# Kernel tuning notes

Measured on AMD Instinct MI355X. Metric: run time of the kernel, lower is better.

The kernel has to match this reference:

```python
import jax, jax.numpy as jnp
import numpy as np

N, M, E, H = 20000, 32, 20, 128


def _branch(nodes, rbf_edges, nbrs_idx, Wf, bf, Wfull, bfull):
    # rbf_edges: [N, M, E] -> edges: [N, M, H]
    edges = rbf_edges @ Wf + bf
    nbrs_fea = nodes[nbrs_idx]  # gather: [N, M, H]
    self_fea = jnp.broadcast_to(nodes[:, None, :], (nbrs_idx.shape[0], nbrs_idx.shape[1], nodes.shape[1]))
    total = jnp.concatenate([self_fea, edges, nbrs_fea], axis=2)  # [N, M, 3H]
    gated = total @ Wfull + bfull  # [N, M, 2H]
    filt, core = gated[..., :H], gated[..., H:]
    return jnp.sum(jax.nn.sigmoid(filt) * jax.nn.softplus(core), axis=1)  # [N, H]


def setup_inputs() -> dict:
    key = jax.random.key(0)
    ks = jax.random.split(key, 12)
    inp = {
        "nodes": jax.random.normal(ks[0], (N, H), jnp.float32),
        "che_rbf_edges": jax.random.normal(ks[1], (N, M, E), jnp.float32),
        "che_nbrs_idx": jax.random.randint(ks[2], (N, M), 0, N),
        "vdw_rbf_edges": jax.random.normal(ks[3], (N, M, E), jnp.float32),
        "vdw_nbrs_idx": jax.random.randint(ks[4], (N, M), 0, N),
        # params (nn.Linear: y = x @ W + b, W stored here as [in, out])
        "che_Wf": jax.random.normal(ks[5], (E, H), jnp.float32) / np.sqrt(E),
        "che_bf": jnp.zeros((H,), jnp.float32),
        "che_Wfull": jax.random.normal(ks[6], (3 * H, 2 * H), jnp.float32) / np.sqrt(3 * H),
        "che_bfull": jnp.zeros((2 * H,), jnp.float32),
        "vdw_Wf": jax.random.normal(ks[7], (E, H), jnp.float32) / np.sqrt(E),
        "vdw_bf": jnp.zeros((H,), jnp.float32),
        "vdw_Wfull": jax.random.normal(ks[8], (3 * H, 2 * H), jnp.float32) / np.sqrt(3 * H),
        "vdw_bfull": jnp.zeros((2 * H,), jnp.float32),
    }
    return inp


def reference(nodes, che_rbf_edges, che_nbrs_idx, vdw_rbf_edges, vdw_nbrs_idx,
              che_Wf, che_bf, che_Wfull, che_bfull,
              vdw_Wf, vdw_bf, vdw_Wfull, vdw_bfull):
    che = _branch(nodes, che_rbf_edges, che_nbrs_idx, che_Wf, che_bf, che_Wfull, che_bfull)
    vdw = _branch(nodes, vdw_rbf_edges, vdw_nbrs_idx, vdw_Wf, vdw_bf, vdw_Wfull, vdw_bfull)
    return jax.nn.softplus(nodes + che + vdw)
```

## Files before the change

kernel.cpp:

```cpp
#include <hip/hip_runtime.h>
#include <hip/hip_bf16.h>

#define NN 20000
#define MM 32
#define EE 20
#define HH 128
#define LOG2E 1.44269504088896f
#define LN2   0.69314718055995f

typedef __attribute__((ext_vector_type(8))) short bf16x8;
typedef __attribute__((ext_vector_type(4))) float f32x4;

__device__ __forceinline__ float bf_lo(unsigned int u) {
    return __uint_as_float(u << 16);
}
__device__ __forceinline__ float bf_hi(unsigned int u) {
    return __uint_as_float(u & 0xFFFF0000u);
}
__device__ __forceinline__ unsigned int pack_bf2(float lo, float hi) {
    unsigned int a = __float_as_uint(lo);
    unsigned int b = __float_as_uint(hi);
    a += 0x7FFFu + ((a >> 16) & 1u);
    b += 0x7FFFu + ((b >> 16) & 1u);
    return (a >> 16) | (b & 0xFFFF0000u);
}
__device__ __forceinline__ unsigned short bf16r(float v) {
    unsigned int u = __float_as_uint(v);
    u += 0x7FFFu + ((u >> 16) & 1u);
    return (unsigned short)(u >> 16);
}
__device__ __forceinline__ float softplusf(float x) {
    return fmaxf(x, 0.f) + __logf(1.f + __expf(-fabsf(x)));
}

__global__ void build_pfrag(const float* __restrict__ cheW,
                            const float* __restrict__ vdwW,
                            unsigned short* __restrict__ Pfrag) {
    int t = blockIdx.x * 256 + threadIdx.x;
    int i = t & 7;
    int l = (t >> 3) & 63;
    int ks = (t >> 9) & 3;
    int tile = t >> 11;
    int j = (tile & 31) * 16 + (l & 15);
    int slot = tile >> 5;
    int b = j >> 8, sec = (j >> 7) & 1, h = j & 127;
    int klocal = (l >> 4) * 8 + i;
    int row = (sec ? 256 : 0) + ks * 32 + klocal;
    const float* W = b ? vdwW : cheW;
    Pfrag[t] = bf16r(LOG2E * W[row * 256 + slot * 128 + h]);
}

__global__ void build_bfrag(const float* __restrict__ cheWf, const float* __restrict__ cheBf,
                            const float* __restrict__ cheW,  const float* __restrict__ cheBfull,
                            const float* __restrict__ vdwWf, const float* __restrict__ vdwBf,
                            const float* __restrict__ vdwW,  const float* __restrict__ vdwBfull,
                            unsigned short* __restrict__ Bfrag, float* __restrict__ biasP) {
    int t = blockIdx.x * 256 + threadIdx.x;
    int b = t >> 10, w = (t >> 9) & 1, tc = (t >> 6) & 7, l = t & 63;
    int lhi = l >> 4, llo = l & 15;
    int h = w * 64 + (tc >> 1) * 16 + llo;
    int slot = tc & 1;
    int jcol = slot * 128 + h;
    const float* Wf = b ? vdwWf : cheWf;
    const float* W  = b ? vdwW  : cheW;

    unsigned short o[8];
#pragma unroll
    for (int i = 0; i < 8; ++i) {
        int k = lhi * 8 + i;
        float a = 0.f;
        if (k < EE)
            for (int h2 = 0; h2 < 128; ++h2)
                a = fmaf(Wf[k * 128 + h2], W[(128 + h2) * 256 + jcol], a);
        o[i] = bf16r(LOG2E * a);
    }
#pragma unroll
    for (int i = 0; i < 8; ++i) Bfrag[t * 8 + i] = o[i];

    if (t < 512) {
        int bb = t >> 8, sl = (t >> 7) & 1, hh = t & 127;
        int jc = sl * 128 + hh;
        const float* bfv   = bb ? vdwBf    : cheBf;
        const float* Wb    = bb ? vdwW     : cheW;
        const float* bfull = bb ? vdwBfull : cheBfull;
        float s = bfull[jc];
        for (int h2 = 0; h2 < 128; ++h2)
            s = fmaf(bfv[h2], Wb[(128 + h2) * 256 + jc], s);
        biasP[t] = LOG2E * s;
    }
}

__global__ __launch_bounds__(256) void proj_mfma(const float* __restrict__ nodes,
                                                 const unsigned short* __restrict__ Pfrag,
                                                 unsigned int* __restrict__ P) {
    __shared__ unsigned short ln[16 * 136];
    int n0 = blockIdx.x * 16;
    int t = threadIdx.x;
    {
        int row = t >> 4, seg = t & 15;
        const float* src = &nodes[(n0 + row) * 128 + seg * 8];
        float4 v0 = *(const float4*)src;
        float4 v1 = *(const float4*)(src + 4);
        uint4 u;
        u.x = pack_bf2(v0.x, v0.y);
        u.y = pack_bf2(v0.z, v0.w);
        u.z = pack_bf2(v1.x, v1.y);
        u.w = pack_bf2(v1.z, v1.w);
        *(uint4*)&ln[row * 136 + seg * 8] = u;
    }
    __syncthreads();

    int w = t >> 6, l = t & 63, lhi = l >> 4, llo = l & 15;
    bf16x8 Af[4];
#pragma unroll
    for (int ks = 0; ks < 4; ++ks)
        Af[ks] = *(const bf16x8*)&ln[llo * 136 + ks * 32 + lhi * 8];

#pragma unroll
    for (int tp = 0; tp < 8; ++tp) {
        int ft = w * 8 + tp;
        int ct = 32 + w * 8 + tp;
        f32x4 cf = {0.f, 0.f, 0.f, 0.f};
        f32x4 cc = {0.f, 0.f, 0.f, 0.f};
#pragma unroll
        for (int ks = 0; ks < 4; ++ks) {
            bf16x8 Bf = *(const bf16x8*)&Pfrag[((ft * 4 + ks) * 64 + l) * 8];
            bf16x8 Bc = *(const bf16x8*)&Pfrag[((ct * 4 + ks) * 64 + l) * 8];
            cf = __builtin_amdgcn_mfma_f32_16x16x32_bf16(Af[ks], Bf, cf, 0, 0, 0);
            cc = __builtin_amdgcn_mfma_f32_16x16x32_bf16(Af[ks], Bc, cc, 0, 0, 0);
        }
        int j = w * 128 + tp * 16 + llo;
#pragma unroll
        for (int r = 0; r < 4; ++r)
            P[(size_t)(n0 + lhi * 4 + r) * 512 + j] = pack_bf2(cf[r], cc[r]);
    }
}

__global__ __launch_bounds__(256) void main_kernel(
    const float* __restrict__ nodes,
    const float* __restrict__ rbf_che, const int* __restrict__ idx_che,
    const float* __restrict__ rbf_vdw, const int* __restrict__ idx_vdw,
    const unsigned int* __restrict__ P,
    const unsigned short* __restrict__ Bfrag, const float* __restrict__ biasP,
    float* __restrict__ out) {
    __shared__ unsigned short sA[2 * 32 * 40];
    __shared__ int sidx[2][MM];
    int n = blockIdx.x;
    int tid = threadIdx.x;
    int w = tid >> 6, l = tid & 63;
    int lhi = l >> 4, llo = l & 15;
    int wold = w >> 1, whalf = w & 1;

    if (tid < 192) {
        int row = tid / 3, j = tid - row * 3;
        *(uint2*)&sA[row * 40 + 20 + j * 4] = make_uint2(0u, 0u);
    }
    for (int i = tid; i < 320; i += 256) {
        int b = (i >= 160) ? 1 : 0, rem = i - b * 160;
        int m = rem / 5, kq = rem - m * 5;
        const float* src = b ? rbf_vdw : rbf_che;
        float4 v = *(const float4*)&src[n * 640 + m * 20 + kq * 4];
        uint2 p;
        p.x = pack_bf2(v.x, v.y);
        p.y = pack_bf2(v.z, v.w);
        *(uint2*)&sA[(b * 32 + m) * 40 + kq * 4] = p;
    }
    if (tid < 64) {
        int b = tid >> 5, m = tid & 31;
        sidx[b][m] = (b ? idx_vdw : idx_che)[n * MM + m];
    }
    __syncthreads();

    float ps0 = 0.f, ps1 = 0.f;

#pragma unroll
    for (int b = 0; b < 2; ++b) {
        bf16x8 Af0 = *(const bf16x8*)&sA[(b * 32 + llo) * 40 + lhi * 8];
        bf16x8 Af1 = *(const bf16x8*)&sA[(b * 32 + 16 + llo) * 40 + lhi * 8];
        int4 vi0 = *(const int4*)&sidx[b][lhi * 4];
        int4 vi1 = *(const int4*)&sidx[b][16 + lhi * 4];

        int secofs = b * 256 + 128 + w * 32 + llo;
        const unsigned int* gp[8];
        gp[0] = P + (size_t)vi0.x * 512 + secofs;
        gp[1] = P + (size_t)vi0.y * 512 + secofs;
        gp[2] = P + (size_t)vi0.z * 512 + secofs;
        gp[3] = P + (size_t)vi0.w * 512 + secofs;
        gp[4] = P + (size_t)vi1.x * 512 + secofs;
        gp[5] = P + (size_t)vi1.y * 512 + secofs;
        gp[6] = P + (size_t)vi1.z * 512 + secofs;
        gp[7] = P + (size_t)vi1.w * 512 + secofs;

        const unsigned int* sp = P + (size_t)n * 512 + b * 256 + w * 32 + llo;
        const float* bfp = biasP + b * 256 + w * 32 + llo;
        const unsigned short* bb = Bfrag + (size_t)((b * 2 + wold) * 8 + whalf * 4) * 512;

#pragma unroll
        for (int ht = 0; ht < 2; ++ht) {
            bf16x8 Bff = *(const bf16x8*)(bb + ((ht * 2) * 64 + l) * 8);
            bf16x8 Bfc = *(const bf16x8*)(bb + ((ht * 2 + 1) * 64 + l) * 8);

            unsigned int su = sp[ht * 16];
            float baseF = bfp[ht * 16]       + bf_lo(su);
            float baseC = bfp[ht * 16 + 128] + bf_hi(su);

            f32x4 a0f = {baseF, baseF, baseF, baseF};
            f32x4 a0c = {baseC, baseC, baseC, baseC};
            f32x4 a1f = a0f, a1c = a0c;
            a0f = __builtin_amdgcn_mfma_f32_16x16x32_bf16(Af0, Bff, a0f, 0, 0, 0);
            a0c = __builtin_amdgcn_mfma_f32_16x16x32_bf16(Af0, Bfc, a0c, 0, 0, 0);
            a1f = __builtin_amdgcn_mfma_f32_16x16x32_bf16(Af1, Bff, a1f, 0, 0, 0);
            a1c = __builtin_amdgcn_mfma_f32_16x16x32_bf16(Af1, Bfc, a1c, 0, 0, 0);

            float s = 0.f;
#pragma unroll
            for (int r = 0; r < 4; ++r) {
                unsigned int g = gp[r][ht * 16];
                float filt = a0f[r] + bf_lo(g);
                float core = a0c[r] + bf_hi(g);
                float sg = __builtin_amdgcn_rcpf(1.f + __builtin_amdgcn_exp2f(-filt));
                float sop = fmaxf(core, 0.f) +
                            __builtin_amdgcn_logf(1.f + __builtin_amdgcn_exp2f(-fabsf(core)));
                s = fmaf(sg, sop, s);
            }
#pragma unroll
            for (int r = 0; r < 4; ++r) {
                unsigned int g = gp[4 + r][ht * 16];
                float filt = a1f[r] + bf_lo(g);
                float core = a1c[r] + bf_hi(g);
                float sg = __builtin_amdgcn_rcpf(1.f + __builtin_amdgcn_exp2f(-filt));
                float sop = fmaxf(core, 0.f) +
                            __builtin_amdgcn_logf(1.f + __builtin_amdgcn_exp2f(-fabsf(core)));
                s = fmaf(sg, sop, s);
            }
            if (ht == 0) ps0 += s;
            else ps1 += s;
        }
    }

    float v0 = ps0;
    v0 += __shfl_xor(v0, 16);
    v0 += __shfl_xor(v0, 32);
    float v1 = ps1;
    v1 += __shfl_xor(v1, 16);
    v1 += __shfl_xor(v1, 32);

    if (lhi < 2) {
        int h = w * 32 + lhi * 16 + llo;
        float res = lhi ? v1 : v0;
        float x = nodes[n * 128 + h] + LN2 * res;
        out[n * 128 + h] = softplusf(x);
    }
}

extern "C" void kernel_launch(void* const* d_in, const int* in_sizes, int n_in,
                              void* d_out, int out_size, void* d_ws, size_t ws_size,
                              hipStream_t stream) {
    const float* nodes     = (const float*)d_in[0];
    const float* che_rbf   = (const float*)d_in[1];
    const int*   che_idx   = (const int*)d_in[2];
    const float* vdw_rbf   = (const float*)d_in[3];
    const int*   vdw_idx   = (const int*)d_in[4];
    const float* che_Wf    = (const float*)d_in[5];
    const float* che_bf    = (const float*)d_in[6];
    const float* che_Wfull = (const float*)d_in[7];
    const float* che_bfull = (const float*)d_in[8];
    const float* vdw_Wf    = (const float*)d_in[9];
    const float* vdw_bf    = (const float*)d_in[10];
    const float* vdw_Wfull = (const float*)d_in[11];
    const float* vdw_bfull = (const float*)d_in[12];

    char* ws = (char*)d_ws;
    unsigned short* Pfrag = (unsigned short*)ws;
    unsigned short* Bfrag = (unsigned short*)(ws + 262144);
    float* biasP          = (float*)(ws + 294912);
    unsigned int* P       = (unsigned int*)(ws + 299008);

    build_pfrag<<<512, 256, 0, stream>>>(che_Wfull, vdw_Wfull, Pfrag);
    build_bfrag<<<8, 256, 0, stream>>>(che_Wf, che_bf, che_Wfull, che_bfull,
                                       vdw_Wf, vdw_bf, vdw_Wfull, vdw_bfull,
                                       Bfrag, biasP);
    proj_mfma<<<NN / 16, 256, 0, stream>>>(nodes, Pfrag, P);
    main_kernel<<<NN, 256, 0, stream>>>(nodes, che_rbf, che_idx, vdw_rbf, vdw_idx,
                                        P, Bfrag, biasP, (float*)d_out);
}
```

Baseline: 175.7 us.

## Make main kernel persistent with double-buffered prefetch of next node's inputs

The main kernel now runs a fixed grid of 2048 blocks, each looping over nodes with a grid stride. It double-buffers the shared-memory rbf tile and neighbour indices, loading the next node's data into registers while the current node is computed. It also simplifies softplus to log(1+exp2(core)), dropping the max/abs stable form, which risks overflow for large core values. This trades away the per-node block launch and exposes global load latency to overlap, at the cost of fewer resident blocks and an extra barrier per iteration.

Result: slower. 290.3 us (+65.2%).

```diff
diff --git a/kernel.cpp b/kernel.cpp
--- a/kernel.cpp
+++ b/kernel.cpp
@@ -5,6 +5,7 @@
 #define MM 32
 #define EE 20
 #define HH 128
+#define GRID 2048
 #define LOG2E 1.44269504088896f
 #define LN2   0.69314718055995f
 
@@ -143,9 +144,9 @@
     const unsigned int* __restrict__ P,
     const unsigned short* __restrict__ Bfrag, const float* __restrict__ biasP,
     float* __restrict__ out) {
-    __shared__ unsigned short sA[2 * 32 * 40];
-    __shared__ int sidx[2][MM];
-    int n = blockIdx.x;
+    __shared__ unsigned short sA[2][2 * 32 * 40];
+    __shared__ int sidx[2][64];
+    int bid = blockIdx.x;
     int tid = threadIdx.x;
     int w = tid >> 6, l = tid & 63;
     int lhi = l >> 4, llo = l & 15;
@@ -153,103 +154,149 @@
 
     if (tid < 192) {
         int row = tid / 3, j = tid - row * 3;
-        *(uint2*)&sA[row * 40 + 20 + j * 4] = make_uint2(0u, 0u);
-    }
-    for (int i = tid; i < 320; i += 256) {
-        int b = (i >= 160) ? 1 : 0, rem = i - b * 160;
-        int m = rem / 5, kq = rem - m * 5;
-        const float* src = b ? rbf_vdw : rbf_che;
-        float4 v = *(const float4*)&src[n * 640 + m * 20 + kq * 4];
+        *(uint2*)&sA[0][row * 40 + 20 + j * 4] = make_uint2(0u, 0u);
+        *(uint2*)&sA[1][row * 40 + 20 + j * 4] = make_uint2(0u, 0u);
+    }
+
+    int i0 = tid;
+    int b0 = i0 >= 160 ? 1 : 0, rem0 = i0 - b0 * 160;
+    int m0 = rem0 / 5, kq0 = rem0 - m0 * 5;
+    int i1 = 256 + tid;
+    int m1 = (i1 - 160) / 5, kq1 = (i1 - 160) - m1 * 5;
+    bool do1 = tid < 64;
+    const float* src0 = b0 ? rbf_vdw : rbf_che;
+
+    float4 v0, v1;
+    int myidx = 0;
+    {
+        v0 = *(const float4*)&src0[bid * 640 + m0 * 20 + kq0 * 4];
+        if (do1) {
+            v1 = *(const float4*)&rbf_vdw[bid * 640 + m1 * 20 + kq1 * 4];
+            myidx = (tid >= 32 ? idx_vdw : idx_che)[bid * MM + (tid & 31)];
+        }
         uint2 p;
-        p.x = pack_bf2(v.x, v.y);
-        p.y = pack_bf2(v.z, v.w);
-        *(uint2*)&sA[(b * 32 + m) * 40 + kq * 4] = p;
-    }
-    if (tid < 64) {
-        int b = tid >> 5, m = tid & 31;
-        sidx[b][m] = (b ? idx_vdw : idx_che)[n * MM + m];
+        p.x = pack_bf2(v0.x, v0.y);
+        p.y = pack_bf2(v0.z, v0.w);
+        *(uint2*)&sA[0][(b0 * 32 + m0) * 40 + kq0 * 4] = p;
+        if (do1) {
+            uint2 q;
+            q.x = pack_bf2(v1.x, v1.y);
+            q.y = pack_bf2(v1.z, v1.w);
+            *(uint2*)&sA[0][(32 + m1) * 40 + kq1 * 4] = q;
+            sidx[0][tid] = myidx;
+        }
     }
     __syncthreads();
 
-    float ps0 = 0.f, ps1 = 0.f;
-
-#pragma unroll
-    for (int b = 0; b < 2; ++b) {
-        bf16x8 Af0 = *(const bf16x8*)&sA[(b * 32 + llo) * 40 + lhi * 8];
-        bf16x8 Af1 = *(const bf16x8*)&sA[(b * 32 + 16 + llo) * 40 + lhi * 8];
-        int4 vi0 = *(const int4*)&sidx[b][lhi * 4];
-        int4 vi1 = *(const int4*)&sidx[b][16 + lhi * 4];
-
-        int secofs = b * 256 + 128 + w * 32 + llo;
-        const unsigned int* gp[8];
-        gp[0] = P + (size_t)vi0.x * 512 + secofs;
-        gp[1] = P + (size_t)vi0.y * 512 + secofs;
-        gp[2] = P + (size_t)vi0.z * 512 + secofs;
-        gp[3] = P + (size_t)vi0.w * 512 + secofs;
-        gp[4] = P + (size_t)vi1.x * 512 + secofs;
-        gp[5] = P + (size_t)vi1.y * 512 + secofs;
-        gp[6] = P + (size_t)vi1.z * 512 + secofs;
-        gp[7] = P + (size_t)vi1.w * 512 + secofs;
-
-        const unsigned int* sp = P + (size_t)n * 512 + b * 256 + w * 32 + llo;
-        const float* bfp = biasP + b * 256 + w * 32 + llo;
-        const unsigned short* bb = Bfrag + (size_t)((b * 2 + wold) * 8 + whalf * 4) * 512;
-
-#pragma unroll
-        for (int ht = 0; ht < 2; ++ht) {
-            bf16x8 Bff = *(const bf16x8*)(bb + ((ht * 2) * 64 + l) * 8);
-            bf16x8 Bfc = *(const bf16x8*)(bb + ((ht * 2 + 1) * 64 + l) * 8);
-
-            unsigned int su = sp[ht * 16];
-            float baseF = bfp[ht * 16]       + bf_lo(su);
-            float baseC = bfp[ht * 16 + 128] + bf_hi(su);
-
-            f32x4 a0f = {baseF, baseF, baseF, baseF};
-            f32x4 a0c = {baseC, baseC, baseC, baseC};
-            f32x4 a1f = a0f, a1c = a0c;
-            a0f = __builtin_amdgcn_mfma_f32_16x16x32_bf16(Af0, Bff, a0f, 0, 0, 0);
-            a0c = __builtin_amdgcn_mfma_f32_16x16x32_bf16(Af0, Bfc, a0c, 0, 0, 0);
-            a1f = __builtin_amdgcn_mfma_f32_16x16x32_bf16(Af1, Bff, a1f, 0, 0, 0);
-            a1c = __builtin_amdgcn_mfma_f32_16x16x32_bf16(Af1, Bfc, a1c, 0, 0, 0);
-
-            float s = 0.f;
-#pragma unroll
-            for (int r = 0; r < 4; ++r) {
-                unsigned int g = gp[r][ht * 16];
-                float filt = a0f[r] + bf_lo(g);
-                float core = a0c[r] + bf_hi(g);
-                float sg = __builtin_amdgcn_rcpf(1.f + __builtin_amdgcn_exp2f(-filt));
-                float sop = fmaxf(core, 0.f) +
-                            __builtin_amdgcn_logf(1.f + __builtin_amdgcn_exp2f(-fabsf(core)));
-                s = fmaf(sg, sop, s);
+    int cur = 0;
+    for (int n = bid; n < NN; n += GRID) {
+        int nn = n + GRID;
+        bool havenext = nn < NN;
+        if (havenext) {
+            v0 = *(const float4*)&src0[nn * 640 + m0 * 20 + kq0 * 4];
+            if (do1) {
+                v1 = *(const float4*)&rbf_vdw[nn * 640 + m1 * 20 + kq1 * 4];
+                myidx = (tid >= 32 ? idx_vdw : idx_che)[nn * MM + (tid & 31)];
             }
-#pragma unroll
-            for (int r = 0; r < 4; ++r) {
-                unsigned int g = gp[4 + r][ht * 16];
-                float filt = a1f[r] + bf_lo(g);
-                float core = a1c[r] + bf_hi(g);
-                float sg = __builtin_amdgcn_rcpf(1.f + __builtin_amdgcn_exp2f(-filt));
-                float sop = fmaxf(core, 0.f) +
-                            __builtin_amdgcn_logf(1.f + __builtin_amdgcn_exp2f(-fabsf(core)));
-                s = fmaf(sg, sop, s);
+        }
+
+        const unsigned short* sAc = sA[cur];
+        const int* sic = sidx[cur];
+        float ps0 = 0.f, ps1 = 0.f;
+
+#pragma unroll
+        for (int b = 0; b < 2; ++b) {
+            bf16x8 Af0 = *(const bf16x8*)&sAc[(b * 32 + llo) * 40 + lhi * 8];
+            bf16x8 Af1 = *(const bf16x8*)&sAc[(b * 32 + 16 + llo) * 40 + lhi * 8];
+            int4 vi0 = *(const int4*)&sic[b * 32 + lhi * 4];
+            int4 vi1 = *(const int4*)&sic[b * 32 + 16 + lhi * 4];
+
+            int secofs = b * 256 + 128 + w * 32 + llo;
+            const unsigned int* gp[8];
+            gp[0] = P + (size_t)vi0.x * 512 + secofs;
+            gp[1] = P + (size_t)vi0.y * 512 + secofs;
+            gp[2] = P + (size_t)vi0.z * 512 + secofs;
+            gp[3] = P + (size_t)vi0.w * 512 + secofs;
+            gp[4] = P + (size_t)vi1.x * 512 + secofs;
+            gp[5] = P + (size_t)vi1.y * 512 + secofs;
+            gp[6] = P + (size_t)vi1.z * 512 + secofs;
+            gp[7] = P + (size_t)vi1.w * 512 + secofs;
+
+            const unsigned int* sp = P + (size_t)n * 512 + b * 256 + w * 32 + llo;
+            const float* bfp = biasP + b * 256 + w * 32 + llo;
+            const unsigned short* bb = Bfrag + (size_t)((b * 2 + wold) * 8 + whalf * 4) * 512;
+
+#pragma unroll
+            for (int ht = 0; ht < 2; ++ht) {
+                bf16x8 Bff = *(const bf16x8*)(bb + ((ht * 2) * 64 + l) * 8);
+                bf16x8 Bfc = *(const bf16x8*)(bb + ((ht * 2 + 1) * 64 + l) * 8);
+
+                unsigned int su = sp[ht * 16];
+                float baseF = bfp[ht * 16]       + bf_lo(su);
+                float baseC = bfp[ht * 16 + 128] + bf_hi(su);
+
+                f32x4 a0f = {baseF, baseF, baseF, baseF};
+                f32x4 a0c = {baseC, baseC, baseC, baseC};
+                f32x4 a1f = a0f, a1c = a0c;
+                a0f = __builtin_amdgcn_mfma_f32_16x16x32_bf16(Af0, Bff, a0f, 0, 0, 0);
+                a0c = __builtin_amdgcn_mfma_f32_16x16x32_bf16(Af0, Bfc, a0c, 0, 0, 0);
+                a1f = __builtin_amdgcn_mfma_f32_16x16x32_bf16(Af1, Bff, a1f, 0, 0, 0);
+                a1c = __builtin_amdgcn_mfma_f32_16x16x32_bf16(Af1, Bfc, a1c, 0, 0, 0);
+
+                float s = 0.f;
+#pragma unroll
+                for (int r = 0; r < 4; ++r) {
+                    unsigned int g = gp[r][ht * 16];
+                    float filt = a0f[r] + bf_lo(g);
+                    float core = a0c[r] + bf_hi(g);
+                    float sg = __builtin_amdgcn_rcpf(1.f + __builtin_amdgcn_exp2f(-filt));
+                    float sop = __builtin_amdgcn_logf(1.f + __builtin_amdgcn_exp2f(core));
+                    s = fmaf(sg, sop, s);
+                }
+#pragma unroll
+                for (int r = 0; r < 4; ++r) {
+                    unsigned int g = gp[4 + r][ht * 16];
+                    float filt = a1f[r] + bf_lo(g);
+                    float core = a1c[r] + bf_hi(g);
+                    float sg = __builtin_amdgcn_rcpf(1.f + __builtin_amdgcn_exp2f(-filt));
+                    float sop = __builtin_amdgcn_logf(1.f + __builtin_amdgcn_exp2f(core));
+                    s = fmaf(sg, sop, s);
+                }
+                if (ht == 0) ps0 += s;
+                else ps1 += s;
             }
-            if (ht == 0) ps0 += s;
-            else ps1 += s;
-        }
-    }
-
-    float v0 = ps0;
-    v0 += __shfl_xor(v0, 16);
-    v0 += __shfl_xor(v0, 32);
-    float v1 = ps1;
-    v1 += __shfl_xor(v1, 16);
-    v1 += __shfl_xor(v1, 32);
-
-    if (lhi < 2) {
-        int h = w * 32 + lhi * 16 + llo;
-        float res = lhi ? v1 : v0;
-        float x = nodes[n * 128 + h] + LN2 * res;
-        out[n * 128 + h] = softplusf(x);
+        }
+
+        float r0 = ps0;
+        r0 += __shfl_xor(r0, 16);
+        r0 += __shfl_xor(r0, 32);
+        float r1 = ps1;
+        r1 += __shfl_xor(r1, 16);
+        r1 += __shfl_xor(r1, 32);
+
+        if (lhi < 2) {
+            int h = w * 32 + lhi * 16 + llo;
+            float res = lhi ? r1 : r0;
+            float x = nodes[n * 128 + h] + LN2 * res;
+            out[n * 128 + h] = softplusf(x);
+        }
+
+        if (havenext) {
+            int nxt = cur ^ 1;
+            uint2 p;
+            p.x = pack_bf2(v0.x, v0.y);
+            p.y = pack_bf2(v0.z, v0.w);
+            *(uint2*)&sA[nxt][(b0 * 32 + m0) * 40 + kq0 * 4] = p;
+            if (do1) {
+                uint2 q;
+                q.x = pack_bf2(v1.x, v1.y);
+                q.y = pack_bf2(v1.z, v1.w);
+                *(uint2*)&sA[nxt][(32 + m1) * 40 + kq1 * 4] = q;
+                sidx[nxt][tid] = myidx;
+            }
+        }
+        __syncthreads();
+        cur ^= 1;
     }
 }
 
@@ -281,6 +328,6 @@
                                        vdw_Wf, vdw_bf, vdw_Wfull, vdw_bfull,
                                        Bfrag, biasP);
     proj_mfma<<<NN / 16, 256, 0, stream>>>(nodes, Pfrag, P);
-    main_kernel<<<NN, 256, 0, stream>>>(nodes, che_rbf, che_idx, vdw_rbf, vdw_idx,
-                                        P, Bfrag, biasP, (float*)d_out);
-}
+    main_kernel<<<GRID, 256, 0, stream>>>(nodes, che_rbf, che_idx, vdw_rbf, vdw_idx,
+                                          P, Bfrag, biasP, (float*)d_out);
+}
```
